# Optimization experiments

Hardware: AMD Instinct MI355X
Metric: run time of the kernel (lower is better)

## Reference

```python
import jax, jax.numpy as jnp
import numpy as np

D_MODEL = 2048
N_HEADS = 16
HEAD_DIM = D_MODEL // N_HEADS


def setup_inputs() -> dict:
    key = jax.random.key(0)
    k_x, k_wqkv, k_bqkv, k_wo, k_bo = jax.random.split(key, 5)
    B, T = 4, 1024
    s_in = 1.0 / np.sqrt(D_MODEL)
    return {
        "x": jax.random.normal(k_x, (B, T, D_MODEL), dtype=jnp.float32),
        "w_qkv": jax.random.uniform(k_wqkv, (D_MODEL, 3 * D_MODEL), jnp.float32, -s_in, s_in),
        "b_qkv": jax.random.uniform(k_bqkv, (3 * D_MODEL,), jnp.float32, -s_in, s_in),
        "w_out": jax.random.uniform(k_wo, (D_MODEL, D_MODEL), jnp.float32, -s_in, s_in),
        "b_out": jax.random.uniform(k_bo, (D_MODEL,), jnp.float32, -s_in, s_in),
    }


def reference(x, w_qkv, b_qkv, w_out, b_out) -> jnp.ndarray:
    B, T, C = x.shape
    qkv = x @ w_qkv + b_qkv                      # [B, T, 3C]
    q, k, v = jnp.split(qkv, 3, axis=-1)
    # [B, H, T, Dh]
    q = q.reshape(B, T, N_HEADS, HEAD_DIM).transpose(0, 2, 1, 3)
    k = k.reshape(B, T, N_HEADS, HEAD_DIM).transpose(0, 2, 1, 3)
    v = v.reshape(B, T, N_HEADS, HEAD_DIM).transpose(0, 2, 1, 3)
    scale = 1.0 / np.sqrt(HEAD_DIM).astype(np.float32)
    att = jnp.einsum("bhqd,bhkd->bhqk", q, k) * scale   # [B, H, T, T]
    causal = jnp.tril(jnp.ones((T, T), dtype=bool))
    att = jnp.where(causal, att, -jnp.inf)
    att = jax.nn.softmax(att, axis=-1)
    out = jnp.einsum("bhqk,bhkd->bhqd", att, v)          # [B, H, T, Dh]
    out = out.transpose(0, 2, 1, 3).reshape(B, T, C)
    return out @ w_out + b_out
```

## Files before the change

kernel.cpp:

```cpp
#include <hip/hip_runtime.h>
#include <hip/hip_bf16.h>
#include <math.h>

#define DM    2048
#define DQKV  6144
#define NH    16
#define DH    128
#define TT    1024
#define BB    4

typedef __bf16 bf16_t;
typedef __bf16 bf16x4 __attribute__((ext_vector_type(4)));
typedef __bf16 bf16x8 __attribute__((ext_vector_type(8)));
typedef float  f32x4  __attribute__((ext_vector_type(4)));

__device__ __forceinline__ void async16(const void* g, void* lds) {
  __builtin_amdgcn_global_load_lds(
      (const __attribute__((address_space(1))) unsigned int*)g,
      (__attribute__((address_space(3))) unsigned int*)lds, 16, 0, 0);
}

__device__ __forceinline__ void block_barrier() {
  asm volatile("" ::: "memory");
  __builtin_amdgcn_s_barrier();
  asm volatile("" ::: "memory");
}

__global__ __launch_bounds__(256) void cast_kernel(const float* __restrict__ X,
                                                   bf16_t* __restrict__ Xb) {
  const size_t i = ((size_t)blockIdx.x * 256 + threadIdx.x) * 8;
  float4 a = *(const float4*)(X + i);
  float4 b = *(const float4*)(X + i + 4);
  bf16x8 o = {(bf16_t)a.x, (bf16_t)a.y, (bf16_t)a.z, (bf16_t)a.w,
              (bf16_t)b.x, (bf16_t)b.y, (bf16_t)b.z, (bf16_t)b.w};
  *(bf16x8*)(Xb + i) = o;
}

__global__ __launch_bounds__(256) void transpose_cast_kernel(
    const float* __restrict__ W, bf16_t* __restrict__ Wt, int K, int N) {
  __shared__ bf16_t tile[64][72];
  const int tid = threadIdx.x;
  const int tk = blockIdx.y * 64, tn = blockIdx.x * 64;
  {
    int r = tid >> 2, c0 = (tid & 3) * 16;
    const float* src = W + (size_t)(tk + r) * N + tn + c0;
#pragma unroll
    for (int j = 0; j < 4; ++j) {
      float4 v = *(const float4*)(src + j * 4);
      tile[r][c0 + j * 4 + 0] = (bf16_t)v.x;
      tile[r][c0 + j * 4 + 1] = (bf16_t)v.y;
      tile[r][c0 + j * 4 + 2] = (bf16_t)v.z;
      tile[r][c0 + j * 4 + 3] = (bf16_t)v.w;
    }
  }
  __syncthreads();
  {
    int n = tid >> 2, c0 = (tid & 3) * 16;
    bf16_t* dst = Wt + (size_t)(tn + n) * K + tk + c0;
#pragma unroll
    for (int j = 0; j < 4; ++j) {
      bf16x4 t = {tile[c0 + j * 4 + 0][n], tile[c0 + j * 4 + 1][n],
                  tile[c0 + j * 4 + 2][n], tile[c0 + j * 4 + 3][n]};
      *(bf16x4*)(dst + j * 4) = t;
    }
  }
}

__global__ __launch_bounds__(256) void v_transpose_kernel(
    const bf16_t* __restrict__ qkv, bf16_t* __restrict__ Vt_g) {
  __shared__ bf16_t tile[64][72];
  const int tid = threadIdx.x;
  const int dt = blockIdx.x;
  const int tt = blockIdx.y;
  const int bh = blockIdx.z;
  const int b = bh >> 4, h = bh & 15;
  {
    int r = tid >> 2, c0 = (tid & 3) * 16;
    const bf16_t* src =
        qkv + (size_t)(b * TT + tt * 64 + r) * DQKV + 2 * DM + h * DH + dt * 64 + c0;
    *(bf16x8*)&tile[r][c0]     = *(const bf16x8*)(src);
    *(bf16x8*)&tile[r][c0 + 8] = *(const bf16x8*)(src + 8);
  }
  __syncthreads();
  {
    int n = tid >> 2, c0 = (tid & 3) * 16;
    bf16_t* dst = Vt_g + (size_t)(bh * DH + dt * 64 + n) * TT + tt * 64 + c0;
#pragma unroll
    for (int j = 0; j < 4; ++j) {
      bf16x4 t = {tile[c0 + j * 4 + 0][n], tile[c0 + j * 4 + 1][n],
                  tile[c0 + j * 4 + 2][n], tile[c0 + j * 4 + 3][n]};
      *(bf16x4*)(dst + j * 4) = t;
    }
  }
}

#define GBM 256
#define GBN 192
template <bool OUT_BF16>
__global__ __launch_bounds__(512, 2) void gemm_big_kernel(
    const bf16_t* __restrict__ A, const bf16_t* __restrict__ Bt,
    const float* __restrict__ bias, void* __restrict__ out,
    int M, int N, int K, int nbm) {
  __shared__ __align__(16) bf16_t As[2][GBM * 64];
  __shared__ __align__(16) bf16_t Bs[2][GBN * 64];

  const int tid  = threadIdx.x;
  const int lane = tid & 63;
  const int wave = tid >> 6;
  const int ln   = lane & 15;
  const int quad = lane >> 4;

  const int cpx = gridDim.x >> 3;
  const int wg  = (blockIdx.x & 7) * cpx + (blockIdx.x >> 3);
  const int bm  = wg & (nbm - 1);
  const int bn  = wg / nbm;

  const bf16_t* Abase = A + (size_t)bm * GBM * K;
  const bf16_t* Bbase = Bt + (size_t)bn * GBN * K;

  const int m0 = (wave >> 2) * 128;
  const int n0 = (wave & 3) * 48;

  f32x4 acc[8][3] = {};

  const int NT = K >> 6;

  auto stageA = [&](int kt, int d) {
#pragma unroll
    for (int s = 0; s < 4; ++s) {
      const int fb  = s * 512 + wave * 64;
      const int f   = fb + lane;
      const int row = f >> 3, c = f & 7;
      const int gc  = c ^ (row & 7);
      async16(Abase + (size_t)row * K + kt * 64 + gc * 8,
              (char*)(&As[d][0]) + fb * 16);
    }
  };
  auto stageB = [&](int kt, int d) {
#pragma unroll
    for (int s = 0; s < 3; ++s) {
      const int fb  = s * 512 + wave * 64;
      const int f   = fb + lane;
      const int row = f >> 3, c = f & 7;
      const int gc  = c ^ (row & 7);
      async16(Bbase + (size_t)row * K + kt * 64 + gc * 8,
              (char*)(&Bs[d][0]) + fb * 16);
    }
  };

  stageA(0, 0);
  stageB(0, 0);
  stageA(1, 1);
  stageB(1, 1);
  asm volatile("s_waitcnt vmcnt(7)" ::: "memory");
  block_barrier();

  for (int kt = 0; kt < NT; ++kt) {
    const int cur = kt & 1;

    bf16x8 af[8][2], bfr[3][2];
#pragma unroll
    for (int ks = 0; ks < 2; ++ks) {
#pragma unroll
      for (int i = 0; i < 8; ++i) {
        const int row = m0 + 16 * i + ln;
        const int c = (ks * 4 + quad) ^ (row & 7);
        af[i][ks] =
            *(const bf16x8*)((const char*)(&As[cur][0]) + ((row * 8 + c) << 4));
      }
#pragma unroll
      for (int j = 0; j < 3; ++j) {
        const int row = n0 + 16 * j + ln;
        const int c = (ks * 4 + quad) ^ (row & 7);
        bfr[j][ks] =
            *(const bf16x8*)((const char*)(&Bs[cur][0]) + ((row * 8 + c) << 4));
      }
    }
    asm volatile("s_waitcnt lgkmcnt(0)" ::: "memory");
    block_barrier();

    if (kt + 2 < NT) stageA(kt + 2, cur);
    __builtin_amdgcn_s_setprio(1);
#pragma unroll
    for (int i = 0; i < 8; ++i)
#pragma unroll
      for (int j = 0; j < 3; ++j)
        acc[i][j] = __builtin_amdgcn_mfma_f32_16x16x32_bf16(af[i][0], bfr[j][0],
                                                            acc[i][j], 0, 0, 0);
    __builtin_amdgcn_s_setprio(0);
    if (kt + 2 < NT) stageB(kt + 2, cur);
    __builtin_amdgcn_s_setprio(1);
#pragma unroll
    for (int i = 0; i < 8; ++i)
#pragma unroll
      for (int j = 0; j < 3; ++j)
        acc[i][j] = __builtin_amdgcn_mfma_f32_16x16x32_bf16(af[i][1], bfr[j][1],
                                                            acc[i][j], 0, 0, 0);
    __builtin_amdgcn_s_setprio(0);

    if (kt + 2 < NT)
      asm volatile("s_waitcnt vmcnt(7)" ::: "memory");
    else
      asm volatile("s_waitcnt vmcnt(0)" ::: "memory");
    block_barrier();
  }

#pragma unroll
  for (int i = 0; i < 8; ++i) {
    const int rowg = bm * GBM + m0 + 16 * i + quad * 4;
#pragma unroll
    for (int j = 0; j < 3; ++j) {
      const int colg = bn * GBN + n0 + 16 * j + ln;
      const float bb = bias[colg];
#pragma unroll
      for (int r = 0; r < 4; ++r) {
        float val = acc[i][j][r] + bb;
        if (OUT_BF16)
          ((bf16_t*)out)[(size_t)(rowg + r) * N + colg] = (bf16_t)val;
        else
          ((float*)out)[(size_t)(rowg + r) * N + colg] = val;
      }
    }
  }
}

__global__ __launch_bounds__(256) void gemm_bt64_kernel(
    const bf16_t* __restrict__ A, const bf16_t* __restrict__ Bt,
    const float* __restrict__ bias, float* __restrict__ out,
    int M, int N, int K) {
  __shared__ __align__(16) bf16_t As[64 * 64];
  __shared__ __align__(16) bf16_t Bs[128 * 64];

  const int tid  = threadIdx.x;
  const int lane = tid & 63;
  const int wave = tid >> 6;
  const int ln   = lane & 15;
  const int quad = lane >> 4;
  const int bm = blockIdx.y, bn = blockIdx.x;
  const int m0 = (wave >> 1) * 32;
  const int n0 = (wave & 1) * 64;

  const bf16_t* Abase = A + (size_t)bm * 64 * K;
  const bf16_t* Bbase = Bt + (size_t)bn * 128 * K;

  f32x4 acc[2][4] = {};

  const int kIters = K >> 6;
  for (int kt = 0; kt < kIters; ++kt) {
    __syncthreads();
#pragma unroll
    for (int j = 0; j < 2; ++j) {
      const int fb  = j * 256 + wave * 64;
      const int f   = fb + lane;
      const int row = f >> 3, c = f & 7;
      const int gc  = c ^ (row & 7);
      async16(Abase + (size_t)row * K + kt * 64 + gc * 8, (char*)As + fb * 16);
    }
#pragma unroll
    for (int j = 0; j < 4; ++j) {
      const int fb  = j * 256 + wave * 64;
      const int f   = fb + lane;
      const int row = f >> 3, c = f & 7;
      const int gc  = c ^ (row & 7);
      async16(Bbase + (size_t)row * K + kt * 64 + gc * 8, (char*)Bs + fb * 16);
    }
    __syncthreads();

#pragma unroll
    for (int ks = 0; ks < 2; ++ks) {
      bf16x8 af[2], bfr[4];
#pragma unroll
      for (int i = 0; i < 2; ++i) {
        int row = m0 + 16 * i + ln;
        int c = (ks * 4 + quad) ^ (row & 7);
        af[i] = *(const bf16x8*)((const char*)As + ((row * 8 + c) << 4));
      }
#pragma unroll
      for (int jj = 0; jj < 4; ++jj) {
        int row = n0 + 16 * jj + ln;
        int c = (ks * 4 + quad) ^ (row & 7);
        bfr[jj] = *(const bf16x8*)((const char*)Bs + ((row * 8 + c) << 4));
      }
#pragma unroll
      for (int i = 0; i < 2; ++i)
#pragma unroll
        for (int jj = 0; jj < 4; ++jj)
          acc[i][jj] = __builtin_amdgcn_mfma_f32_16x16x32_bf16(
              af[i], bfr[jj], acc[i][jj], 0, 0, 0);
    }
  }

#pragma unroll
  for (int i = 0; i < 2; ++i) {
    int rowg = bm * 64 + m0 + 16 * i + quad * 4;
#pragma unroll
    for (int j = 0; j < 4; ++j) {
      int colg = bn * 128 + n0 + 16 * j + ln;
      float bb = bias[colg];
#pragma unroll
      for (int r = 0; r < 4; ++r)
        out[(size_t)(rowg + r) * N + colg] = acc[i][j][r] + bb;
    }
  }
}

__global__ __launch_bounds__(256, 4) void attn_kernel(
    const bf16_t* __restrict__ qkv, const bf16_t* __restrict__ Vt_g,
    bf16_t* __restrict__ attout) {
  const int bx = blockIdx.x;
  const int bh = bx & 63;
  const int qt = 15 - (bx >> 6);
  const int b  = bh >> 4;
  const int h  = bh & 15;
  const int tid  = threadIdx.x;
  const int lane = tid & 63;
  const int wave = tid >> 6;
  const int ln   = lane & 15;
  const int quad = lane >> 4;

  __shared__ __align__(16) bf16_t Ks[64 * 128];
  __shared__ __align__(16) bf16_t Vs[128 * 64];
  __shared__ __align__(16) bf16_t Ps[4 * 16 * 64];

  const float scale = 0.08838834764831845f;
  const float SHIFT = 12.0f;
  const int q0 = qt * 64 + wave * 16;

  bf16x8 aq[4];
  {
    const bf16_t* qrow = qkv + (size_t)(b * TT + q0 + ln) * DQKV + h * DH;
#pragma unroll
    for (int kt = 0; kt < 4; ++kt)
      aq[kt] = *(const bf16x8*)(qrow + kt * 32 + quad * 8);
  }

  f32x4 o[8] = {};
  float lp[4] = {0.f, 0.f, 0.f, 0.f};

  for (int c = 0; c <= qt; ++c) {
    const int kc = c * 64;
    __syncthreads();

#pragma unroll
    for (int j = 0; j < 4; ++j) {
      const int fb = j * 256 + wave * 64;
      const int l  = fb + lane;
      {
        const int row = l >> 4, cc = l & 15;
        const int gc  = cc ^ (row & 7);
        const bf16_t* g =
            qkv + (size_t)(b * TT + kc + row) * DQKV + DM + h * DH + gc * 8;
        async16(g, (char*)Ks + fb * 16);
      }
      {
        const int d = l >> 3, cc = l & 7;
        const int gc = cc ^ (d & 7);
        const bf16_t* g = Vt_g + (size_t)(bh * DH + d) * TT + kc + gc * 8;
        async16(g, (char*)Vs + fb * 16);
      }
    }
    __syncthreads();

    f32x4 sacc[4];
#pragma unroll
    for (int jt = 0; jt < 4; ++jt) {
      sacc[jt] = (f32x4){0.f, 0.f, 0.f, 0.f};
#pragma unroll
      for (int kt = 0; kt < 4; ++kt) {
        const int row = jt * 16 + ln;
        const int sc  = (kt * 4 + quad) ^ (row & 7);
        bf16x8 bk = *(const bf16x8*)((const char*)Ks + row * 256 + sc * 16);
        sacc[jt] = __builtin_amdgcn_mfma_f32_16x16x32_bf16(aq[kt], bk,
                                                           sacc[jt], 0, 0, 0);
      }
    }

    const bool diag = (c == qt);
#pragma unroll
    for (int jt = 0; jt < 4; ++jt) {
      const int colg = kc + jt * 16 + ln;
#pragma unroll
      for (int r = 0; r < 4; ++r) {
        float sv = sacc[jt][r] * scale - SHIFT;
        if (diag && colg > q0 + quad * 4 + r) sv = -1e30f;
        float pv = __expf(sv);
        lp[r] += pv;
        const int row = quad * 4 + r;
        const int col = jt * 16 + ln;
        const int sc  = (col >> 3) ^ (row & 7);
        Ps[wave * 1024 + row * 64 + sc * 8 + (col & 7)] = (bf16_t)pv;
      }
    }

#pragma unroll
    for (int ks = 0; ks < 2; ++ks) {
      const int psc = (ks * 4 + quad) ^ (ln & 7);
      bf16x8 ap =
          *(const bf16x8*)((const char*)Ps + wave * 2048 + ln * 128 + psc * 16);
#pragma unroll
      for (int nt = 0; nt < 8; ++nt) {
        const int row = nt * 16 + ln;
        const int sc  = (ks * 4 + quad) ^ (row & 7);
        bf16x8 bv = *(const bf16x8*)((const char*)Vs + row * 128 + sc * 16);
        o[nt] = __builtin_amdgcn_mfma_f32_16x16x32_bf16(ap, bv, o[nt], 0, 0, 0);
      }
    }
  }

#pragma unroll
  for (int off = 1; off < 16; off <<= 1)
#pragma unroll
    for (int r = 0; r < 4; ++r) lp[r] += __shfl_xor(lp[r], off, 64);

#pragma unroll
  for (int r = 0; r < 4; ++r) {
    float inv = 1.0f / lp[r];
    int t = q0 + quad * 4 + r;
    bf16_t* orow = attout + (size_t)(b * TT + t) * DM + h * DH;
#pragma unroll
    for (int nt = 0; nt < 8; ++nt)
      orow[nt * 16 + ln] = (bf16_t)(o[nt][r] * inv);
  }
}

extern "C" void kernel_launch(void* const* d_in, const int* in_sizes, int n_in,
                              void* d_out, int out_size, void* d_ws,
                              size_t ws_size, hipStream_t stream) {
  const float* x     = (const float*)d_in[0];
  const float* w_qkv = (const float*)d_in[1];
  const float* b_qkv = (const float*)d_in[2];
  const float* w_out = (const float*)d_in[3];
  const float* b_out = (const float*)d_in[4];
  float* out = (float*)d_out;

  char* ws = (char*)d_ws;
  bf16_t* qkv    = (bf16_t*)(ws);
  bf16_t* wqkv_t = (bf16_t*)(ws + 50331648);
  bf16_t* Vt_g   = wqkv_t;
  bf16_t* wout_t = (bf16_t*)(ws + 75497472);
  bf16_t* xb     = (bf16_t*)(ws + 83886080);
  bf16_t* attout = xb;

  dim3 blk(256);
  cast_kernel<<<dim3(4096), blk, 0, stream>>>(x, xb);
  transpose_cast_kernel<<<dim3(96, 32), blk, 0, stream>>>(w_qkv, wqkv_t, 2048, 6144);
  transpose_cast_kernel<<<dim3(32, 32), blk, 0, stream>>>(w_out, wout_t, 2048, 2048);
  gemm_big_kernel<true><<<dim3(512), dim3(512), 0, stream>>>(
      xb, wqkv_t, b_qkv, qkv, 4096, 6144, 2048, 16);
  v_transpose_kernel<<<dim3(2, 16, 64), blk, 0, stream>>>(qkv, Vt_g);
  attn_kernel<<<dim3(1024), blk, 0, stream>>>(qkv, Vt_g, attout);
  gemm_bt64_kernel
      <<<dim3(16, 64), blk, 0, stream>>>(attout, wout_t, b_out, out, 4096, 2048, 2048);
}
```

Measured before the change: 339.4 us.

## Split GEMM mainloop into four phases with interleaved chunk-ordered async staging

Reworks the big GEMM mainloop into four phases per k-tile, one per k-half and M-half. Each phase loads only its own A/B fragments, issues a subset of the next tile's async global-to-LDS copies, then runs its MFMAs. Staging is ordered so the A row chunks a phase needs arrive first, which allows finer vmcnt waits, and global pointers are precomputed and advanced by stride instead of recomputed. The goal is better overlap of memory traffic with MFMA work and lower fragment register pressure. The cost is more barriers per tile, and the prefetch distance drops from two tiles to one.

```diff
diff --git a/kernel.cpp b/kernel.cpp
--- a/kernel.cpp
+++ b/kernel.cpp
@@ -96,6 +96,40 @@
 
 #define GBM 256
 #define GBN 192
+
+#define VM2 asm volatile("s_waitcnt vmcnt(2)" ::: "memory")
+#define VM0 asm volatile("s_waitcnt vmcnt(0)" ::: "memory")
+#define NOWAIT ((void)0)
+#define NOSTAGE ((void)0)
+
+#define PHASE(KS, MH, STAGE, WAIT)                                          \
+  {                                                                         \
+    bf16x8 af[4];                                                           \
+    _Pragma("unroll") for (int i = 0; i < 4; ++i) {                         \
+      const int row = m0 + (MH) * 64 + 16 * i + ln;                         \
+      const int cc = ((KS) * 4 + quad) ^ (row & 7);                         \
+      af[i] = *(const bf16x8*)(curA + ((row * 8 + cc) << 4));               \
+    }                                                                       \
+    if ((MH) == 0) {                                                        \
+      _Pragma("unroll") for (int j = 0; j < 3; ++j) {                       \
+        const int row = n0 + 16 * j + ln;                                   \
+        const int cc = ((KS) * 4 + quad) ^ (row & 7);                       \
+        bfr[j] = *(const bf16x8*)(curB + ((row * 8 + cc) << 4));            \
+      }                                                                     \
+    }                                                                       \
+    STAGE;                                                                  \
+    block_barrier();                                                        \
+    __builtin_amdgcn_s_setprio(1);                                          \
+    _Pragma("unroll") for (int i = 0; i < 4; ++i)                           \
+      _Pragma("unroll") for (int j = 0; j < 3; ++j)                         \
+        acc[(MH) * 4 + i][j] = __builtin_amdgcn_mfma_f32_16x16x32_bf16(     \
+            af[i], bfr[j], acc[(MH) * 4 + i][j], 0, 0, 0);                  \
+    __builtin_amdgcn_s_setprio(0);                                          \
+    __builtin_amdgcn_sched_barrier(0);                                      \
+    WAIT;                                                                   \
+    block_barrier();                                                        \
+  }
+
 template <bool OUT_BF16>
 __global__ __launch_bounds__(512, 2) void gemm_big_kernel(
     const bf16_t* __restrict__ A, const bf16_t* __restrict__ Bt,
@@ -125,84 +159,74 @@
 
   const int NT = K >> 6;
 
-  auto stageA = [&](int kt, int d) {
-#pragma unroll
-    for (int s = 0; s < 4; ++s) {
-      const int fb  = s * 512 + wave * 64;
-      const int f   = fb + lane;
-      const int row = f >> 3, c = f & 7;
-      const int gc  = c ^ (row & 7);
-      async16(Abase + (size_t)row * K + kt * 64 + gc * 8,
-              (char*)(&As[d][0]) + fb * 16);
-    }
+  const bf16_t* gA[4];
+#pragma unroll
+  for (int s = 0; s < 4; ++s) {
+    const int f = s * 512 + tid;
+    const int row = f >> 3, c = f & 7;
+    const int gc = c ^ (row & 7);
+    gA[s] = Abase + (size_t)row * K + gc * 8;
+  }
+  const bf16_t* gB[3];
+#pragma unroll
+  for (int s = 0; s < 3; ++s) {
+    const int f = s * 512 + tid;
+    const int row = f >> 3, c = f & 7;
+    const int gc = c ^ (row & 7);
+    gB[s] = Bbase + (size_t)row * K + gc * 8;
+  }
+
+  auto stA = [&](int s, char* base) {
+    async16(gA[s], base + (size_t)((s * 512 + wave * 64) * 16));
   };
-  auto stageB = [&](int kt, int d) {
-#pragma unroll
-    for (int s = 0; s < 3; ++s) {
-      const int fb  = s * 512 + wave * 64;
-      const int f   = fb + lane;
-      const int row = f >> 3, c = f & 7;
-      const int gc  = c ^ (row & 7);
-      async16(Bbase + (size_t)row * K + kt * 64 + gc * 8,
-              (char*)(&Bs[d][0]) + fb * 16);
-    }
+  auto stB = [&](int s, char* base) {
+    async16(gB[s], base + (size_t)((s * 512 + wave * 64) * 16));
   };
-
-  stageA(0, 0);
-  stageB(0, 0);
-  stageA(1, 1);
-  stageB(1, 1);
-  asm volatile("s_waitcnt vmcnt(7)" ::: "memory");
-  block_barrier();
-
-  for (int kt = 0; kt < NT; ++kt) {
+  auto fence = [&] { asm volatile("" ::: "memory"); };
+  auto adv = [&] {
+#pragma unroll
+    for (int s = 0; s < 4; ++s) gA[s] += 64;
+#pragma unroll
+    for (int s = 0; s < 3; ++s) gB[s] += 64;
+  };
+
+  {
+    char* bA = (char*)(&As[0][0]);
+    char* bB = (char*)(&Bs[0][0]);
+    stA(0, bA); fence();
+    stA(2, bA); fence();
+    stB(0, bB); fence();
+    stB(1, bB); fence();
+    stB(2, bB); fence();
+    stA(1, bA); fence();
+    stA(3, bA);
+    adv();
+    VM2;
+    block_barrier();
+  }
+
+  for (int kt = 0; kt < NT - 1; ++kt) {
     const int cur = kt & 1;
-
-    bf16x8 af[8][2], bfr[3][2];
-#pragma unroll
-    for (int ks = 0; ks < 2; ++ks) {
-#pragma unroll
-      for (int i = 0; i < 8; ++i) {
-        const int row = m0 + 16 * i + ln;
-        const int c = (ks * 4 + quad) ^ (row & 7);
-        af[i][ks] =
-            *(const bf16x8*)((const char*)(&As[cur][0]) + ((row * 8 + c) << 4));
-      }
-#pragma unroll
-      for (int j = 0; j < 3; ++j) {
-        const int row = n0 + 16 * j + ln;
-        const int c = (ks * 4 + quad) ^ (row & 7);
-        bfr[j][ks] =
-            *(const bf16x8*)((const char*)(&Bs[cur][0]) + ((row * 8 + c) << 4));
-      }
-    }
-    asm volatile("s_waitcnt lgkmcnt(0)" ::: "memory");
-    block_barrier();
-
-    if (kt + 2 < NT) stageA(kt + 2, cur);
-    __builtin_amdgcn_s_setprio(1);
-#pragma unroll
-    for (int i = 0; i < 8; ++i)
-#pragma unroll
-      for (int j = 0; j < 3; ++j)
-        acc[i][j] = __builtin_amdgcn_mfma_f32_16x16x32_bf16(af[i][0], bfr[j][0],
-                                                            acc[i][j], 0, 0, 0);
-    __builtin_amdgcn_s_setprio(0);
-    if (kt + 2 < NT) stageB(kt + 2, cur);
-    __builtin_amdgcn_s_setprio(1);
-#pragma unroll
-    for (int i = 0; i < 8; ++i)
-#pragma unroll
-      for (int j = 0; j < 3; ++j)
-        acc[i][j] = __builtin_amdgcn_mfma_f32_16x16x32_bf16(af[i][1], bfr[j][1],
-                                                            acc[i][j], 0, 0, 0);
-    __builtin_amdgcn_s_setprio(0);
-
-    if (kt + 2 < NT)
-      asm volatile("s_waitcnt vmcnt(7)" ::: "memory");
-    else
-      asm volatile("s_waitcnt vmcnt(0)" ::: "memory");
-    block_barrier();
+    const char* curA = (const char*)(&As[cur][0]);
+    const char* curB = (const char*)(&Bs[cur][0]);
+    char* nA = (char*)(&As[cur ^ 1][0]);
+    char* nB = (char*)(&Bs[cur ^ 1][0]);
+    bf16x8 bfr[3];
+    PHASE(0, 0, (stA(0, nA), stA(2, nA)), VM2);
+    PHASE(0, 1, (stB(0, nB), stB(1, nB)), NOWAIT);
+    PHASE(1, 0, (stB(2, nB), fence(), stA(1, nA)), NOWAIT);
+    PHASE(1, 1, (stA(3, nA)), VM2);
+    adv();
+  }
+  {
+    const int cur = (NT - 1) & 1;
+    const char* curA = (const char*)(&As[cur][0]);
+    const char* curB = (const char*)(&Bs[cur][0]);
+    bf16x8 bfr[3];
+    PHASE(0, 0, NOSTAGE, VM0);
+    PHASE(0, 1, NOSTAGE, NOWAIT);
+    PHASE(1, 0, NOSTAGE, NOWAIT);
+    PHASE(1, 1, NOSTAGE, NOWAIT);
   }
 
 #pragma unroll
```

New measurement: 370.2 us. 1.09x slower.

## Double-buffer attention K/V tiles and reuse the big pipelined GEMM for the output projection

Applied to the files above, without the earlier changes.

The attention kernel now double-buffers K and V tiles in LDS, prefetching the next key chunk while computing the current one, and raises MFMA priority around the matrix-multiply phases. Occupancy is lowered to 2 blocks per CU because of the larger LDS footprint. The output projection switches from a simple single-buffered 64x128 tile GEMM to the templated 256x128 double-buffered GEMM kernel, launching 256 workgroups. The risk is lower attention occupancy and fewer workgroups than CUs in the output GEMM.

```diff
diff --git a/kernel.cpp b/kernel.cpp
--- a/kernel.cpp
+++ b/kernel.cpp
@@ -94,15 +94,13 @@
   }
 }
 
-#define GBM 256
-#define GBN 192
-template <bool OUT_BF16>
+template <bool OUT_BF16, int BCH>
 __global__ __launch_bounds__(512, 2) void gemm_big_kernel(
     const bf16_t* __restrict__ A, const bf16_t* __restrict__ Bt,
     const float* __restrict__ bias, void* __restrict__ out,
     int M, int N, int K, int nbm) {
-  __shared__ __align__(16) bf16_t As[2][GBM * 64];
-  __shared__ __align__(16) bf16_t Bs[2][GBN * 64];
+  __shared__ __align__(16) bf16_t As[2][256 * 64];
+  __shared__ __align__(16) bf16_t Bs[2][BCH * 64 * 64];
 
   const int tid  = threadIdx.x;
   const int lane = tid & 63;
@@ -115,13 +113,13 @@
   const int bm  = wg & (nbm - 1);
   const int bn  = wg / nbm;
 
-  const bf16_t* Abase = A + (size_t)bm * GBM * K;
-  const bf16_t* Bbase = Bt + (size_t)bn * GBN * K;
+  const bf16_t* Abase = A + (size_t)bm * 256 * K;
+  const bf16_t* Bbase = Bt + (size_t)bn * (BCH * 64) * K;
 
   const int m0 = (wave >> 2) * 128;
-  const int n0 = (wave & 3) * 48;
-
-  f32x4 acc[8][3] = {};
+  const int n0 = (wave & 3) * (BCH * 16);
+
+  f32x4 acc[8][BCH] = {};
 
   const int NT = K >> 6;
 
@@ -138,7 +136,7 @@
   };
   auto stageB = [&](int kt, int d) {
 #pragma unroll
-    for (int s = 0; s < 3; ++s) {
+    for (int s = 0; s < BCH; ++s) {
       const int fb  = s * 512 + wave * 64;
       const int f   = fb + lane;
       const int row = f >> 3, c = f & 7;
@@ -147,18 +145,24 @@
               (char*)(&Bs[d][0]) + fb * 16);
     }
   };
+  auto vm_lpt = [&] {
+    if constexpr (BCH == 3)
+      asm volatile("s_waitcnt vmcnt(7)" ::: "memory");
+    else
+      asm volatile("s_waitcnt vmcnt(6)" ::: "memory");
+  };
 
   stageA(0, 0);
   stageB(0, 0);
   stageA(1, 1);
   stageB(1, 1);
-  asm volatile("s_waitcnt vmcnt(7)" ::: "memory");
+  vm_lpt();
   block_barrier();
 
   for (int kt = 0; kt < NT; ++kt) {
     const int cur = kt & 1;
 
-    bf16x8 af[8][2], bfr[3][2];
+    bf16x8 af[8][2], bfr[BCH][2];
 #pragma unroll
     for (int ks = 0; ks < 2; ++ks) {
 #pragma unroll
@@ -169,7 +173,7 @@
             *(const bf16x8*)((const char*)(&As[cur][0]) + ((row * 8 + c) << 4));
       }
 #pragma unroll
-      for (int j = 0; j < 3; ++j) {
+      for (int j = 0; j < BCH; ++j) {
         const int row = n0 + 16 * j + ln;
         const int c = (ks * 4 + quad) ^ (row & 7);
         bfr[j][ks] =
@@ -184,7 +188,7 @@
 #pragma unroll
     for (int i = 0; i < 8; ++i)
 #pragma unroll
-      for (int j = 0; j < 3; ++j)
+      for (int j = 0; j < BCH; ++j)
         acc[i][j] = __builtin_amdgcn_mfma_f32_16x16x32_bf16(af[i][0], bfr[j][0],
                                                             acc[i][j], 0, 0, 0);
     __builtin_amdgcn_s_setprio(0);
@@ -193,13 +197,13 @@
 #pragma unroll
     for (int i = 0; i < 8; ++i)
 #pragma unroll
-      for (int j = 0; j < 3; ++j)
+      for (int j = 0; j < BCH; ++j)
         acc[i][j] = __builtin_amdgcn_mfma_f32_16x16x32_bf16(af[i][1], bfr[j][1],
                                                             acc[i][j], 0, 0, 0);
     __builtin_amdgcn_s_setprio(0);
 
     if (kt + 2 < NT)
-      asm volatile("s_waitcnt vmcnt(7)" ::: "memory");
+      vm_lpt();
     else
       asm volatile("s_waitcnt vmcnt(0)" ::: "memory");
     block_barrier();
@@ -207,10 +211,10 @@
 
 #pragma unroll
   for (int i = 0; i < 8; ++i) {
-    const int rowg = bm * GBM + m0 + 16 * i + quad * 4;
-#pragma unroll
-    for (int j = 0; j < 3; ++j) {
-      const int colg = bn * GBN + n0 + 16 * j + ln;
+    const int rowg = bm * 256 + m0 + 16 * i + quad * 4;
+#pragma unroll
+    for (int j = 0; j < BCH; ++j) {
+      const int colg = bn * (BCH * 64) + n0 + 16 * j + ln;
       const float bb = bias[colg];
 #pragma unroll
       for (int r = 0; r < 4; ++r) {
@@ -224,87 +228,7 @@
   }
 }
 
-__global__ __launch_bounds__(256) void gemm_bt64_kernel(
-    const bf16_t* __restrict__ A, const bf16_t* __restrict__ Bt,
-    const float* __restrict__ bias, float* __restrict__ out,
-    int M, int N, int K) {
-  __shared__ __align__(16) bf16_t As[64 * 64];
-  __shared__ __align__(16) bf16_t Bs[128 * 64];
-
-  const int tid  = threadIdx.x;
-  const int lane = tid & 63;
-  const int wave = tid >> 6;
-  const int ln   = lane & 15;
-  const int quad = lane >> 4;
-  const int bm = blockIdx.y, bn = blockIdx.x;
-  const int m0 = (wave >> 1) * 32;
-  const int n0 = (wave & 1) * 64;
-
-  const bf16_t* Abase = A + (size_t)bm * 64 * K;
-  const bf16_t* Bbase = Bt + (size_t)bn * 128 * K;
-
-  f32x4 acc[2][4] = {};
-
-  const int kIters = K >> 6;
-  for (int kt = 0; kt < kIters; ++kt) {
-    __syncthreads();
-#pragma unroll
-    for (int j = 0; j < 2; ++j) {
-      const int fb  = j * 256 + wave * 64;
-      const int f   = fb + lane;
-      const int row = f >> 3, c = f & 7;
-      const int gc  = c ^ (row & 7);
-      async16(Abase + (size_t)row * K + kt * 64 + gc * 8, (char*)As + fb * 16);
-    }
-#pragma unroll
-    for (int j = 0; j < 4; ++j) {
-      const int fb  = j * 256 + wave * 64;
-      const int f   = fb + lane;
-      const int row = f >> 3, c = f & 7;
-      const int gc  = c ^ (row & 7);
-      async16(Bbase + (size_t)row * K + kt * 64 + gc * 8, (char*)Bs + fb * 16);
-    }
-    __syncthreads();
-
-#pragma unroll
-    for (int ks = 0; ks < 2; ++ks) {
-      bf16x8 af[2], bfr[4];
-#pragma unroll
-      for (int i = 0; i < 2; ++i) {
-        int row = m0 + 16 * i + ln;
-        int c = (ks * 4 + quad) ^ (row & 7);
-        af[i] = *(const bf16x8*)((const char*)As + ((row * 8 + c) << 4));
-      }
-#pragma unroll
-      for (int jj = 0; jj < 4; ++jj) {
-        int row = n0 + 16 * jj + ln;
-        int c = (ks * 4 + quad) ^ (row & 7);
-        bfr[jj] = *(const bf16x8*)((const char*)Bs + ((row * 8 + c) << 4));
-      }
-#pragma unroll
-      for (int i = 0; i < 2; ++i)
-#pragma unroll
-        for (int jj = 0; jj < 4; ++jj)
-          acc[i][jj] = __builtin_amdgcn_mfma_f32_16x16x32_bf16(
-              af[i], bfr[jj], acc[i][jj], 0, 0, 0);
-    }
-  }
-
-#pragma unroll
-  for (int i = 0; i < 2; ++i) {
-    int rowg = bm * 64 + m0 + 16 * i + quad * 4;
-#pragma unroll
-    for (int j = 0; j < 4; ++j) {
-      int colg = bn * 128 + n0 + 16 * j + ln;
-      float bb = bias[colg];
-#pragma unroll
-      for (int r = 0; r < 4; ++r)
-        out[(size_t)(rowg + r) * N + colg] = acc[i][j][r] + bb;
-    }
-  }
-}
-
-__global__ __launch_bounds__(256, 4) void attn_kernel(
+__global__ __launch_bounds__(256, 2) void attn_kernel(
     const bf16_t* __restrict__ qkv, const bf16_t* __restrict__ Vt_g,
     bf16_t* __restrict__ attout) {
   const int bx = blockIdx.x;
@@ -318,8 +242,8 @@
   const int ln   = lane & 15;
   const int quad = lane >> 4;
 
-  __shared__ __align__(16) bf16_t Ks[64 * 128];
-  __shared__ __align__(16) bf16_t Vs[128 * 64];
+  __shared__ __align__(16) bf16_t Ks[2][64 * 128];
+  __shared__ __align__(16) bf16_t Vs[2][128 * 64];
   __shared__ __align__(16) bf16_t Ps[4 * 16 * 64];
 
   const float scale = 0.08838834764831845f;
@@ -334,13 +258,8 @@
       aq[kt] = *(const bf16x8*)(qrow + kt * 32 + quad * 8);
   }
 
-  f32x4 o[8] = {};
-  float lp[4] = {0.f, 0.f, 0.f, 0.f};
-
-  for (int c = 0; c <= qt; ++c) {
+  auto stage = [&](int c, int buf) {
     const int kc = c * 64;
-    __syncthreads();
-
 #pragma unroll
     for (int j = 0; j < 4; ++j) {
       const int fb = j * 256 + wave * 64;
@@ -350,18 +269,39 @@
         const int gc  = cc ^ (row & 7);
         const bf16_t* g =
             qkv + (size_t)(b * TT + kc + row) * DQKV + DM + h * DH + gc * 8;
-        async16(g, (char*)Ks + fb * 16);
+        async16(g, (char*)(&Ks[buf][0]) + fb * 16);
       }
       {
         const int d = l >> 3, cc = l & 7;
         const int gc = cc ^ (d & 7);
         const bf16_t* g = Vt_g + (size_t)(bh * DH + d) * TT + kc + gc * 8;
-        async16(g, (char*)Vs + fb * 16);
-      }
-    }
-    __syncthreads();
+        async16(g, (char*)(&Vs[buf][0]) + fb * 16);
+      }
+    }
+  };
+
+  f32x4 o[8] = {};
+  float lp[4] = {0.f, 0.f, 0.f, 0.f};
+
+  stage(0, 0);
+
+  for (int c = 0; c <= qt; ++c) {
+    const int cur = c & 1;
+    const char* Kc = (const char*)(&Ks[cur][0]);
+    const char* Vc = (const char*)(&Vs[cur][0]);
+
+    asm volatile("s_waitcnt lgkmcnt(0)" ::: "memory");
+    block_barrier();
+    if (c < qt) {
+      stage(c + 1, cur ^ 1);
+      asm volatile("s_waitcnt vmcnt(8)" ::: "memory");
+    } else {
+      asm volatile("s_waitcnt vmcnt(0)" ::: "memory");
+    }
+    block_barrier();
 
     f32x4 sacc[4];
+    __builtin_amdgcn_s_setprio(1);
 #pragma unroll
     for (int jt = 0; jt < 4; ++jt) {
       sacc[jt] = (f32x4){0.f, 0.f, 0.f, 0.f};
@@ -369,12 +309,14 @@
       for (int kt = 0; kt < 4; ++kt) {
         const int row = jt * 16 + ln;
         const int sc  = (kt * 4 + quad) ^ (row & 7);
-        bf16x8 bk = *(const bf16x8*)((const char*)Ks + row * 256 + sc * 16);
+        bf16x8 bk = *(const bf16x8*)(Kc + row * 256 + sc * 16);
         sacc[jt] = __builtin_amdgcn_mfma_f32_16x16x32_bf16(aq[kt], bk,
                                                            sacc[jt], 0, 0, 0);
       }
     }
-
+    __builtin_amdgcn_s_setprio(0);
+
+    const int kc = c * 64;
     const bool diag = (c == qt);
 #pragma unroll
     for (int jt = 0; jt < 4; ++jt) {
@@ -392,6 +334,7 @@
       }
     }
 
+    __builtin_amdgcn_s_setprio(1);
 #pragma unroll
     for (int ks = 0; ks < 2; ++ks) {
       const int psc = (ks * 4 + quad) ^ (ln & 7);
@@ -401,10 +344,11 @@
       for (int nt = 0; nt < 8; ++nt) {
         const int row = nt * 16 + ln;
         const int sc  = (ks * 4 + quad) ^ (row & 7);
-        bf16x8 bv = *(const bf16x8*)((const char*)Vs + row * 128 + sc * 16);
+        bf16x8 bv = *(const bf16x8*)(Vc + row * 128 + sc * 16);
         o[nt] = __builtin_amdgcn_mfma_f32_16x16x32_bf16(ap, bv, o[nt], 0, 0, 0);
       }
     }
+    __builtin_amdgcn_s_setprio(0);
   }
 
 #pragma unroll
@@ -445,10 +389,10 @@
   cast_kernel<<<dim3(4096), blk, 0, stream>>>(x, xb);
   transpose_cast_kernel<<<dim3(96, 32), blk, 0, stream>>>(w_qkv, wqkv_t, 2048, 6144);
   transpose_cast_kernel<<<dim3(32, 32), blk, 0, stream>>>(w_out, wout_t, 2048, 2048);
-  gemm_big_kernel<true><<<dim3(512), dim3(512), 0, stream>>>(
+  gemm_big_kernel<true, 3><<<dim3(512), dim3(512), 0, stream>>>(
       xb, wqkv_t, b_qkv, qkv, 4096, 6144, 2048, 16);
   v_transpose_kernel<<<dim3(2, 16, 64), blk, 0, stream>>>(qkv, Vt_g);
   attn_kernel<<<dim3(1024), blk, 0, stream>>>(qkv, Vt_g, attout);
-  gemm_bt64_kernel
-      <<<dim3(16, 64), blk, 0, stream>>>(attout, wout_t, b_out, out, 4096, 2048, 2048);
-}
+  gemm_big_kernel<false, 2><<<dim3(256), dim3(512), 0, stream>>>(
+      attout, wout_t, b_out, out, 4096, 2048, 2048, 16);
+}
```

Measured after the change: 333.6 us. About the same (-1.7%).
